# Optimization experiments

Measured on AMD Instinct MI355X. Metric: run time of the kernel, lower is better.

The kernel has to match this reference:

```python
import jax, jax.numpy as jnp
import numpy as np
from jax import lax


def _conv(x, w):
    # x: [B,H,W,C], w: [kh,kw,Cin,Cout], stride 1, 'same' padding
    return lax.conv_general_dilated(x, w, window_strides=(1, 1), padding='SAME',
                                    dimension_numbers=('NHWC', 'HWIO', 'NHWC'))


def setup_inputs() -> dict:
    key = jax.random.key(0)
    ks = jax.random.split(key, 4)
    B, T, H, W, Cin, F = 16, 5, 256, 256, 3, 8
    return {
        'input_tensor': jax.random.normal(ks[0], (B, T, H, W, Cin), jnp.float32),
        'kernel': jax.random.normal(ks[1], (3, 3, Cin, 4 * F), jnp.float32) * 0.1,
        'recurrent_kernel': jax.random.normal(ks[2], (3, 3, F, 4 * F), jnp.float32) * 0.1,
        'bias': jnp.zeros((4 * F,), jnp.float32),
        'gamma': jnp.ones((F,), jnp.float32),
        'beta': jnp.zeros((F,), jnp.float32),
        'moving_mean': jnp.zeros((F,), jnp.float32),
        'moving_var': jnp.ones((F,), jnp.float32),
        'dense_w': jax.random.normal(ks[3], (F, 2), jnp.float32) * 0.1,
        'dense_b': jnp.zeros((2,), jnp.float32),
    }


def reference(input_tensor, kernel, recurrent_kernel, bias, gamma, beta,
              moving_mean, moving_var, dense_w, dense_b):
    B, T, H, W, Cin = input_tensor.shape
    F = recurrent_kernel.shape[2]
    xs = jnp.moveaxis(input_tensor, 1, 0)  # [T,B,H,W,Cin] time-major for scan
    h0 = jnp.zeros((B, H, W, F), input_tensor.dtype)

    def step(carry, x_t):
        h, c = carry
        # fused 4-gate pre-activations, Keras gate order: i, f, c(g), o
        z = _conv(x_t, kernel) + _conv(h, recurrent_kernel) + bias
        i, f, g, o = jnp.split(z, 4, axis=-1)
        i = jax.nn.sigmoid(i)
        f = jax.nn.sigmoid(f)
        g = jnp.tanh(g)
        o = jax.nn.sigmoid(o)
        c = f * c + i * g
        h = o * jnp.tanh(c)
        return (h, c), None

    (h, _), _ = lax.scan(step, (h0, h0), xs)  # return_sequences=False -> last h

    # BatchNormalization (inference, Keras eps=1e-3)
    eps = 1e-3
    x = (h - moving_mean) * lax.rsqrt(moving_var + eps) * gamma + beta
    # LeakyReLU, Keras default alpha=0.3
    x = jnp.where(x >= 0, x, 0.3 * x)
    # Dense(2) over channel dim
    return jnp.einsum('bhwf,fk->bhwk', x, dense_w) + dense_b
```

## Files before the change

### kernel.cpp

```cpp
#include <hip/hip_runtime.h>


#define BB  16
#define TT  5
#define HH  256
#define WW  256
#define CIN 3
#define FF  8
#define GG  32

#define TW  32
#define THT 16
#define LW  34
#define LH  18

typedef _Float16 half8 __attribute__((ext_vector_type(8)));
typedef _Float16 half4 __attribute__((ext_vector_type(4)));
typedef float    floatx4 __attribute__((ext_vector_type(4)));

__device__ __forceinline__ float frcp(float x) { return __builtin_amdgcn_rcpf(x); }
__device__ __forceinline__ float fsig(float x) { return frcp(1.0f + __expf(-x)); }
__device__ __forceinline__ float ftanh_(float x) { return 1.0f - 2.0f * frcp(1.0f + __expf(2.0f * x)); }

#define MFMA(A, B, C) __builtin_amdgcn_mfma_f32_16x16x32_f16((A), (B), (C), 0, 0, 0)

__global__ void build_frags(const float* __restrict__ wk,
                            const float* __restrict__ wr,
                            _Float16* __restrict__ blob) {
    const int lane = threadIdx.x & 63;
    const int quad = lane >> 4, nlo = lane & 15;
    for (int chunk = 0; chunk < 5; ++chunk) {
        for (int nh = 0; nh < 2; ++nh) {
            const int n = nh * 16 + nlo;
            const int frag = chunk * 2 + nh;
            _Float16* dhi = blob + ((size_t)frag * 64 + lane) * 8;
            _Float16* dlo = blob + ((size_t)(10 + frag) * 64 + lane) * 8;
            for (int j = 0; j < 8; ++j) {
                const int k = quad * 8 + j;
                float w = 0.0f;
                if (chunk == 0) {
                    int tap = k >> 2, ci = k & 3;
                    if (ci < 3) w = wk[(tap * 3 + ci) * GG + n];
                } else if (chunk == 1) {
                    if (quad == 0 && j < 3) w = wk[(8 * 3 + j) * GG + n];
                } else {
                    int c = chunk - 2;
                    int tap = c * 4 + quad, ci = j;
                    if (tap < 9) w = wr[(tap * FF + ci) * GG + n];
                }
                _Float16 wh = (_Float16)w;
                dhi[j] = wh;
                dlo[j] = (_Float16)(w - (float)wh);
            }
        }
    }
}

template <bool FIRST>
__global__ __launch_bounds__(256) void lstm_step(
    const float* __restrict__ xg,
    int t,
    const _Float16* __restrict__ blob,
    const float* __restrict__ bias,
    const _Float16* __restrict__ hin,
    _Float16* __restrict__ hout,
    float* __restrict__ cbuf)
{
    __shared__ half8 hls[LH * LW];
    __shared__ half4 xh_ls[LH * LW];
    __shared__ half4 xl_ls[LH * LW];

    const int tid  = threadIdx.x;
    const int bx = blockIdx.x, by = blockIdx.y, b = blockIdx.z;
    const int lane = tid & 63, wave = tid >> 6;
    const int quad = lane >> 4, nlo = lane & 15;

    half8 bfh[10], bfl[10];
#pragma unroll
    for (int i = 0; i < 10; ++i) {
        bfh[i] = *(const half8*)(blob + ((size_t)i * 64 + lane) * 8);
        bfl[i] = *(const half8*)(blob + ((size_t)(10 + i) * 64 + lane) * 8);
    }
    const float bv0 = bias[nlo], bv1 = bias[16 + nlo];

    for (int l = tid; l < LH * LW; l += 256) {
        int r = l / LW, c = l - r * LW;
        int gy = by * THT + r - 1, gx = bx * TW + c - 1;
        half4 vh = {(_Float16)0, (_Float16)0, (_Float16)0, (_Float16)0};
        half4 vl = vh;
        if ((unsigned)gy < HH && (unsigned)gx < WW) {
            const float* p = xg + (((size_t)(b * TT + t) * HH + gy) * WW + gx) * CIN;
#pragma unroll
            for (int ch = 0; ch < 3; ++ch) {
                float xv = p[ch];
                _Float16 xh = (_Float16)xv;
                vh[ch] = xh;
                vl[ch] = (_Float16)(xv - (float)xh);
            }
        }
        xh_ls[l] = vh;
        xl_ls[l] = vl;
    }
    if (!FIRST) {
        for (int l = tid; l < LH * LW; l += 256) {
            int r = l / LW, c = l - r * LW;
            int gy = by * THT + r - 1, gx = bx * TW + c - 1;
            half8 v = {(_Float16)0, (_Float16)0, (_Float16)0, (_Float16)0,
                       (_Float16)0, (_Float16)0, (_Float16)0, (_Float16)0};
            if ((unsigned)gy < HH && (unsigned)gx < WW)
                v = *(const half8*)(hin + ((size_t)(b * HH + gy) * WW + gx) * FF);
            hls[l] = v;
        }
    }
    __syncthreads();

    const int gidbase = (((b * gridDim.y + by) * gridDim.x + bx) * 4 + wave) * 8;

    for (int g = 0; g < 8; ++g) {
        const int lr  = wave * 4 + (g >> 1);
        const int gx0 = (g & 1) * 16;
        const int lc  = gx0 + nlo;

        const int t0 = 2 * quad, t1 = t0 + 1;
        const int i0 = (lr + t0 / 3) * LW + lc + t0 % 3;
        const int i1 = (lr + t1 / 3) * LW + lc + t1 % 3;
        const int i2 = (lr + 2) * LW + lc + 2;
        half8 a_xA_h, a_xB_h, a_xA_l, a_xB_l;
        {
            half4 p = xh_ls[i0], q = xh_ls[i1], s = xh_ls[i2];
            a_xA_h = (half8){p.x, p.y, p.z, p.w, q.x, q.y, q.z, q.w};
            a_xB_h = (half8){s.x, s.y, s.z, s.w, s.x, s.y, s.z, s.w};
        }
        {
            half4 p = xl_ls[i0], q = xl_ls[i1], s = xl_ls[i2];
            a_xA_l = (half8){p.x, p.y, p.z, p.w, q.x, q.y, q.z, q.w};
            a_xB_l = (half8){s.x, s.y, s.z, s.w, s.x, s.y, s.z, s.w};
        }

        floatx4 acc0 = {bv0, bv0, bv0, bv0};
        floatx4 acc1 = {bv1, bv1, bv1, bv1};
        acc0 = MFMA(a_xA_h, bfh[0], acc0);  acc1 = MFMA(a_xA_h, bfh[1], acc1);
        acc0 = MFMA(a_xB_h, bfh[2], acc0);  acc1 = MFMA(a_xB_h, bfh[3], acc1);
        acc0 = MFMA(a_xA_l, bfh[0], acc0);  acc1 = MFMA(a_xA_l, bfh[1], acc1);
        acc0 = MFMA(a_xB_l, bfh[2], acc0);  acc1 = MFMA(a_xB_l, bfh[3], acc1);
        acc0 = MFMA(a_xA_h, bfl[0], acc0);  acc1 = MFMA(a_xA_h, bfl[1], acc1);
        acc0 = MFMA(a_xB_h, bfl[2], acc0);  acc1 = MFMA(a_xB_h, bfl[3], acc1);
        if (!FIRST) {
#pragma unroll
            for (int c = 0; c < 3; ++c) {
                int tap = c * 4 + quad;
                if (tap > 8) tap = 8;
                half8 ah = hls[(lr + tap / 3) * LW + lc + tap % 3];
                acc0 = MFMA(ah, bfh[4 + c * 2], acc0);
                acc1 = MFMA(ah, bfh[5 + c * 2], acc1);
                acc0 = MFMA(ah, bfl[4 + c * 2], acc0);
                acc1 = MFMA(ah, bfl[5 + c * 2], acc1);
            }
        }

        const bool lo8 = (nlo < 8);
        float s0 = lo8 ? acc0[2] : acc0[0]; float r0 = __shfl_xor(s0, 8, 64);
        float s1 = lo8 ? acc0[3] : acc0[1]; float r1 = __shfl_xor(s1, 8, 64);
        float s2 = lo8 ? acc1[2] : acc1[0]; float r2 = __shfl_xor(s2, 8, 64);
        float s3 = lo8 ? acc1[3] : acc1[1]; float r3 = __shfl_xor(s3, 8, 64);

        const float zi0 = lo8 ? acc0[0] : r0, zi1 = lo8 ? acc0[1] : r1;
        const float zf0 = lo8 ? r0 : acc0[2], zf1 = lo8 ? r1 : acc0[3];
        const float zg0 = lo8 ? acc1[0] : r2, zg1 = lo8 ? acc1[1] : r3;
        const float zo0 = lo8 ? r2 : acc1[2], zo1 = lo8 ? r3 : acc1[3];

        float* cp = cbuf + ((size_t)(gidbase + g) * 64 + lane) * 2;
        float c0 = 0.0f, c1 = 0.0f;
        if (!FIRST) { float2 cc = *(const float2*)cp; c0 = cc.x; c1 = cc.y; }

        const float ii0 = fsig(zi0), ff0 = fsig(zf0), gg0 = ftanh_(zg0), oo0 = fsig(zo0);
        const float cn0 = ff0 * c0 + ii0 * gg0;
        const float hn0 = oo0 * ftanh_(cn0);
        const float ii1 = fsig(zi1), ff1 = fsig(zf1), gg1 = ftanh_(zg1), oo1 = fsig(zo1);
        const float cn1 = ff1 * c1 + ii1 * gg1;
        const float hn1 = oo1 * ftanh_(cn1);
        *(float2*)cp = make_float2(cn0, cn1);

        const int fc = nlo & 7;
        const int m0 = quad * 4 + (lo8 ? 0 : 2);
        const int gy = by * THT + lr;
        _Float16* hp = hout + ((size_t)(b * HH + gy) * WW + bx * TW + gx0 + m0) * FF + fc;
        hp[0]  = (_Float16)hn0;
        hp[FF] = (_Float16)hn1;
    }
}

__global__ __launch_bounds__(256) void epilogue_kernel(
    const _Float16* __restrict__ hbuf,
    const float* __restrict__ gamma, const float* __restrict__ beta,
    const float* __restrict__ mean,  const float* __restrict__ var,
    const float* __restrict__ dw,    const float* __restrict__ db,
    float* __restrict__ out)
{
    const size_t p = (size_t)blockIdx.x * 256 + threadIdx.x;
    half8 hv8 = *(const half8*)(hbuf + p * FF);
    float o0 = db[0], o1 = db[1];
#pragma unroll
    for (int f = 0; f < FF; ++f) {
        float s = gamma[f] * rsqrtf(var[f] + 1e-3f);
        float x = ((float)hv8[f] - mean[f]) * s + beta[f];
        x = (x >= 0.f) ? x : 0.3f * x;
        o0 = fmaf(x, dw[f * 2 + 0], o0);
        o1 = fmaf(x, dw[f * 2 + 1], o1);
    }
    *(float2*)(out + p * 2) = make_float2(o0, o1);
}

extern "C" void kernel_launch(void* const* d_in, const int* in_sizes, int n_in,
                              void* d_out, int out_size, void* d_ws, size_t ws_size,
                              hipStream_t stream) {
    const float* x     = (const float*)d_in[0];
    const float* wk    = (const float*)d_in[1];
    const float* wr    = (const float*)d_in[2];
    const float* bias  = (const float*)d_in[3];
    const float* gamma = (const float*)d_in[4];
    const float* beta  = (const float*)d_in[5];
    const float* mean  = (const float*)d_in[6];
    const float* var   = (const float*)d_in[7];
    const float* dw    = (const float*)d_in[8];
    const float* db    = (const float*)d_in[9];
    float* out = (float*)d_out;

    const size_t state = (size_t)BB * HH * WW * FF;
    _Float16* blob = (_Float16*)d_ws;
    float*    cbuf = (float*)((char*)d_ws + 32768);
    _Float16* h0   = (_Float16*)((char*)d_ws + 32768 + state * 4);
    _Float16* h1   = (_Float16*)((char*)h0 + state * 2);

    build_frags<<<1, 64, 0, stream>>>(wk, wr, blob);

    dim3 grid(WW / TW, HH / THT, BB);
    dim3 block(256);
    _Float16* bufs[2] = {h0, h1};
    lstm_step<true><<<grid, block, 0, stream>>>(x, 0, blob, bias, h0 , bufs[1], cbuf);
    for (int t = 1; t < TT; ++t)
        lstm_step<false><<<grid, block, 0, stream>>>(x, t, blob, bias, bufs[t & 1], bufs[(t + 1) & 1], cbuf);

    epilogue_kernel<<<(BB * HH * WW) / 256, 256, 0, stream>>>(
        bufs[TT & 1], gamma, beta, mean, var, dw, db, out);
}
```

Baseline: 276.7 us.

## Fuse all LSTM timesteps and epilogue into one persistent kernel with grid barriers

Replaces the per-timestep kernel launches and the separate epilogue with a single persistent kernel of 512 blocks. Each block owns two 32x32 tiles across all timesteps and synchronises between steps with an atomic grid barrier. The cell state now lives in registers instead of a global buffer, and BN, LeakyReLU and Dense are fused into the last step. It also drops the low-half split of the input x (fp16 only), which removes MFMAs but loses precision, and the co-residency needed by the grid barrier raises register pressure and deadlock risk.

Measured after the change: 989.7 us. 3.58x slower.

```diff
diff --git a/kernel.cpp b/kernel.cpp
--- a/kernel.cpp
+++ b/kernel.cpp
@@ -10,9 +10,11 @@
 #define GG  32
 
 #define TW  32
-#define THT 16
+#define THT 32
 #define LW  34
-#define LH  18
+#define LH  34
+#define NG  16
+#define NBLK 512
 
 typedef _Float16 half8 __attribute__((ext_vector_type(8)));
 typedef _Float16 half4 __attribute__((ext_vector_type(4)));
@@ -56,52 +58,50 @@
     }
 }
 
-template <bool FIRST>
-__global__ __launch_bounds__(256) void lstm_step(
+__device__ __forceinline__ void grid_barrier(unsigned* cnt) {
+    __syncthreads();
+    __threadfence();
+    if (threadIdx.x == 0) {
+        __hip_atomic_fetch_add(cnt, 1u, __ATOMIC_ACQ_REL, __HIP_MEMORY_SCOPE_AGENT);
+        while (__hip_atomic_load(cnt, __ATOMIC_ACQUIRE, __HIP_MEMORY_SCOPE_AGENT)
+               < (unsigned)NBLK)
+            __builtin_amdgcn_s_sleep(8);
+    }
+    __syncthreads();
+    __threadfence();
+}
+
+__device__ __forceinline__ void process_tile(
+    int t, int tile,
     const float* __restrict__ xg,
-    int t,
-    const _Float16* __restrict__ blob,
-    const float* __restrict__ bias,
-    const _Float16* __restrict__ hin,
-    _Float16* __restrict__ hout,
-    float* __restrict__ cbuf)
+    const half8 (&bfh)[10], const half8 (&bfl)[10],
+    float bv0, float bv1,
+    float bn_s, float bn_b, float dw0, float dw1, float db0, float db1,
+    const _Float16* __restrict__ hin, _Float16* __restrict__ hout,
+    float* __restrict__ out,
+    half8* hls, half4* xls,
+    float (&creg)[NG][2])
 {
-    __shared__ half8 hls[LH * LW];
-    __shared__ half4 xh_ls[LH * LW];
-    __shared__ half4 xl_ls[LH * LW];
-
     const int tid  = threadIdx.x;
-    const int bx = blockIdx.x, by = blockIdx.y, b = blockIdx.z;
+    const int b = tile >> 6, by = (tile >> 3) & 7, bx = tile & 7;
     const int lane = tid & 63, wave = tid >> 6;
     const int quad = lane >> 4, nlo = lane & 15;
-
-    half8 bfh[10], bfl[10];
-#pragma unroll
-    for (int i = 0; i < 10; ++i) {
-        bfh[i] = *(const half8*)(blob + ((size_t)i * 64 + lane) * 8);
-        bfl[i] = *(const half8*)(blob + ((size_t)(10 + i) * 64 + lane) * 8);
-    }
-    const float bv0 = bias[nlo], bv1 = bias[16 + nlo];
+    const bool lo8 = (nlo < 8);
+    const int fc = nlo & 7;
+
+    __syncthreads();
 
     for (int l = tid; l < LH * LW; l += 256) {
         int r = l / LW, c = l - r * LW;
         int gy = by * THT + r - 1, gx = bx * TW + c - 1;
         half4 vh = {(_Float16)0, (_Float16)0, (_Float16)0, (_Float16)0};
-        half4 vl = vh;
         if ((unsigned)gy < HH && (unsigned)gx < WW) {
             const float* p = xg + (((size_t)(b * TT + t) * HH + gy) * WW + gx) * CIN;
-#pragma unroll
-            for (int ch = 0; ch < 3; ++ch) {
-                float xv = p[ch];
-                _Float16 xh = (_Float16)xv;
-                vh[ch] = xh;
-                vl[ch] = (_Float16)(xv - (float)xh);
-            }
-        }
-        xh_ls[l] = vh;
-        xl_ls[l] = vl;
-    }
-    if (!FIRST) {
+            vh.x = (_Float16)p[0]; vh.y = (_Float16)p[1]; vh.z = (_Float16)p[2];
+        }
+        xls[l] = vh;
+    }
+    if (t > 0) {
         for (int l = tid; l < LH * LW; l += 256) {
             int r = l / LW, c = l - r * LW;
             int gy = by * THT + r - 1, gx = bx * TW + c - 1;
@@ -114,38 +114,26 @@
     }
     __syncthreads();
 
-    const int gidbase = (((b * gridDim.y + by) * gridDim.x + bx) * 4 + wave) * 8;
-
-    for (int g = 0; g < 8; ++g) {
-        const int lr  = wave * 4 + (g >> 1);
+#pragma unroll
+    for (int g = 0; g < NG; ++g) {
+        const int lr  = wave * 8 + (g >> 1);
         const int gx0 = (g & 1) * 16;
         const int lc  = gx0 + nlo;
 
         const int t0 = 2 * quad, t1 = t0 + 1;
-        const int i0 = (lr + t0 / 3) * LW + lc + t0 % 3;
-        const int i1 = (lr + t1 / 3) * LW + lc + t1 % 3;
-        const int i2 = (lr + 2) * LW + lc + 2;
-        half8 a_xA_h, a_xB_h, a_xA_l, a_xB_l;
-        {
-            half4 p = xh_ls[i0], q = xh_ls[i1], s = xh_ls[i2];
-            a_xA_h = (half8){p.x, p.y, p.z, p.w, q.x, q.y, q.z, q.w};
-            a_xB_h = (half8){s.x, s.y, s.z, s.w, s.x, s.y, s.z, s.w};
-        }
-        {
-            half4 p = xl_ls[i0], q = xl_ls[i1], s = xl_ls[i2];
-            a_xA_l = (half8){p.x, p.y, p.z, p.w, q.x, q.y, q.z, q.w};
-            a_xB_l = (half8){s.x, s.y, s.z, s.w, s.x, s.y, s.z, s.w};
-        }
+        half4 p = xls[(lr + t0 / 3) * LW + lc + t0 % 3];
+        half4 q = xls[(lr + t1 / 3) * LW + lc + t1 % 3];
+        half4 s = xls[(lr + 2) * LW + lc + 2];
+        half8 a_xA = (half8){p.x, p.y, p.z, p.w, q.x, q.y, q.z, q.w};
+        half8 a_xB = (half8){s.x, s.y, s.z, s.w, s.x, s.y, s.z, s.w};
 
         floatx4 acc0 = {bv0, bv0, bv0, bv0};
         floatx4 acc1 = {bv1, bv1, bv1, bv1};
-        acc0 = MFMA(a_xA_h, bfh[0], acc0);  acc1 = MFMA(a_xA_h, bfh[1], acc1);
-        acc0 = MFMA(a_xB_h, bfh[2], acc0);  acc1 = MFMA(a_xB_h, bfh[3], acc1);
-        acc0 = MFMA(a_xA_l, bfh[0], acc0);  acc1 = MFMA(a_xA_l, bfh[1], acc1);
-        acc0 = MFMA(a_xB_l, bfh[2], acc0);  acc1 = MFMA(a_xB_l, bfh[3], acc1);
-        acc0 = MFMA(a_xA_h, bfl[0], acc0);  acc1 = MFMA(a_xA_h, bfl[1], acc1);
-        acc0 = MFMA(a_xB_h, bfl[2], acc0);  acc1 = MFMA(a_xB_h, bfl[3], acc1);
-        if (!FIRST) {
+        acc0 = MFMA(a_xA, bfh[0], acc0);  acc1 = MFMA(a_xA, bfh[1], acc1);
+        acc0 = MFMA(a_xB, bfh[2], acc0);  acc1 = MFMA(a_xB, bfh[3], acc1);
+        acc0 = MFMA(a_xA, bfl[0], acc0);  acc1 = MFMA(a_xA, bfl[1], acc1);
+        acc0 = MFMA(a_xB, bfl[2], acc0);  acc1 = MFMA(a_xB, bfl[3], acc1);
+        if (t > 0) {
 #pragma unroll
             for (int c = 0; c < 3; ++c) {
                 int tap = c * 4 + quad;
@@ -158,7 +146,6 @@
             }
         }
 
-        const bool lo8 = (nlo < 8);
         float s0 = lo8 ? acc0[2] : acc0[0]; float r0 = __shfl_xor(s0, 8, 64);
         float s1 = lo8 ? acc0[3] : acc0[1]; float r1 = __shfl_xor(s1, 8, 64);
         float s2 = lo8 ? acc1[2] : acc1[0]; float r2 = __shfl_xor(s2, 8, 64);
@@ -169,46 +156,92 @@
         const float zg0 = lo8 ? acc1[0] : r2, zg1 = lo8 ? acc1[1] : r3;
         const float zo0 = lo8 ? r2 : acc1[2], zo1 = lo8 ? r3 : acc1[3];
 
-        float* cp = cbuf + ((size_t)(gidbase + g) * 64 + lane) * 2;
-        float c0 = 0.0f, c1 = 0.0f;
-        if (!FIRST) { float2 cc = *(const float2*)cp; c0 = cc.x; c1 = cc.y; }
-
         const float ii0 = fsig(zi0), ff0 = fsig(zf0), gg0 = ftanh_(zg0), oo0 = fsig(zo0);
-        const float cn0 = ff0 * c0 + ii0 * gg0;
+        const float cn0 = ff0 * creg[g][0] + ii0 * gg0;
         const float hn0 = oo0 * ftanh_(cn0);
         const float ii1 = fsig(zi1), ff1 = fsig(zf1), gg1 = ftanh_(zg1), oo1 = fsig(zo1);
-        const float cn1 = ff1 * c1 + ii1 * gg1;
+        const float cn1 = ff1 * creg[g][1] + ii1 * gg1;
         const float hn1 = oo1 * ftanh_(cn1);
-        *(float2*)cp = make_float2(cn0, cn1);
-
-        const int fc = nlo & 7;
+        creg[g][0] = cn0; creg[g][1] = cn1;
+
         const int m0 = quad * 4 + (lo8 ? 0 : 2);
         const int gy = by * THT + lr;
-        _Float16* hp = hout + ((size_t)(b * HH + gy) * WW + bx * TW + gx0 + m0) * FF + fc;
-        hp[0]  = (_Float16)hn0;
-        hp[FF] = (_Float16)hn1;
-    }
-}
-
-__global__ __launch_bounds__(256) void epilogue_kernel(
-    const _Float16* __restrict__ hbuf,
+        if (t < TT - 1) {
+            _Float16* hp = hout + ((size_t)(b * HH + gy) * WW + bx * TW + gx0 + m0) * FF + fc;
+            hp[0]  = (_Float16)hn0;
+            hp[FF] = (_Float16)hn1;
+        } else {
+            float y0 = bn_s * hn0 + bn_b; y0 = (y0 >= 0.f) ? y0 : 0.3f * y0;
+            float y1 = bn_s * hn1 + bn_b; y1 = (y1 >= 0.f) ? y1 : 0.3f * y1;
+            float p00 = y0 * dw0, p01 = y0 * dw1;
+            float p10 = y1 * dw0, p11 = y1 * dw1;
+#pragma unroll
+            for (int m = 1; m <= 4; m <<= 1) {
+                p00 += __shfl_xor(p00, m, 64);
+                p01 += __shfl_xor(p01, m, 64);
+                p10 += __shfl_xor(p10, m, 64);
+                p11 += __shfl_xor(p11, m, 64);
+            }
+            const int j = nlo & 7;
+            if (j < 4) {
+                const int px = m0 + (j >> 1);
+                const int k  = j & 1;
+                float val = (j == 0 ? p00 : j == 1 ? p01 : j == 2 ? p10 : p11)
+                            + (k ? db1 : db0);
+                out[((size_t)(b * HH + gy) * WW + bx * TW + gx0 + px) * 2 + k] = val;
+            }
+        }
+    }
+}
+
+__global__ __launch_bounds__(256, 3) void lstm_all(
+    const float* __restrict__ xg,
+    const _Float16* __restrict__ blob,
+    const float* __restrict__ bias,
     const float* __restrict__ gamma, const float* __restrict__ beta,
     const float* __restrict__ mean,  const float* __restrict__ var,
     const float* __restrict__ dw,    const float* __restrict__ db,
-    float* __restrict__ out)
+    _Float16* __restrict__ h0g, _Float16* __restrict__ h1g,
+    float* __restrict__ out, unsigned* __restrict__ barcnt)
 {
-    const size_t p = (size_t)blockIdx.x * 256 + threadIdx.x;
-    half8 hv8 = *(const half8*)(hbuf + p * FF);
-    float o0 = db[0], o1 = db[1];
-#pragma unroll
-    for (int f = 0; f < FF; ++f) {
-        float s = gamma[f] * rsqrtf(var[f] + 1e-3f);
-        float x = ((float)hv8[f] - mean[f]) * s + beta[f];
-        x = (x >= 0.f) ? x : 0.3f * x;
-        o0 = fmaf(x, dw[f * 2 + 0], o0);
-        o1 = fmaf(x, dw[f * 2 + 1], o1);
-    }
-    *(float2*)(out + p * 2) = make_float2(o0, o1);
+    __shared__ half8 hls[LH * LW];
+    __shared__ half4 xls[LH * LW];
+
+    const int lane = threadIdx.x & 63;
+    const int nlo = lane & 15, fc = nlo & 7;
+
+    half8 bfh[10], bfl[10];
+#pragma unroll
+    for (int i = 0; i < 10; ++i) {
+        bfh[i] = *(const half8*)(blob + ((size_t)i * 64 + lane) * 8);
+        bfl[i] = *(const half8*)(blob + ((size_t)(10 + i) * 64 + lane) * 8);
+    }
+    const float bv0 = bias[nlo], bv1 = bias[16 + nlo];
+    const float bn_s = gamma[fc] * rsqrtf(var[fc] + 1e-3f);
+    const float bn_b = beta[fc] - mean[fc] * bn_s;
+    const float dw0 = dw[fc * 2 + 0], dw1 = dw[fc * 2 + 1];
+    const float db0 = db[0], db1 = db[1];
+
+    float cregA[NG][2], cregB[NG][2];
+#pragma unroll
+    for (int g = 0; g < NG; ++g) {
+        cregA[g][0] = 0.f; cregA[g][1] = 0.f;
+        cregB[g][0] = 0.f; cregB[g][1] = 0.f;
+    }
+
+    for (int t = 0; t < TT; ++t) {
+        const _Float16* hin = (t & 1) ? h0g : h1g;
+        _Float16* hout      = (t & 1) ? h1g : h0g;
+
+        process_tile(t, (int)blockIdx.x, xg, bfh, bfl, bv0, bv1,
+                     bn_s, bn_b, dw0, dw1, db0, db1,
+                     hin, hout, out, hls, xls, cregA);
+        process_tile(t, (int)blockIdx.x + NBLK, xg, bfh, bfl, bv0, bv1,
+                     bn_s, bn_b, dw0, dw1, db0, db1,
+                     hin, hout, out, hls, xls, cregB);
+
+        if (t < TT - 1) grid_barrier(barcnt + t * 16);
+    }
 }
 
 extern "C" void kernel_launch(void* const* d_in, const int* in_sizes, int n_in,
@@ -227,20 +260,14 @@
     float* out = (float*)d_out;
 
     const size_t state = (size_t)BB * HH * WW * FF;
-    _Float16* blob = (_Float16*)d_ws;
-    float*    cbuf = (float*)((char*)d_ws + 32768);
-    _Float16* h0   = (_Float16*)((char*)d_ws + 32768 + state * 4);
-    _Float16* h1   = (_Float16*)((char*)h0 + state * 2);
-
+    _Float16* blob   = (_Float16*)d_ws;
+    unsigned* barcnt = (unsigned*)((char*)d_ws + 24576);
+    _Float16* h0     = (_Float16*)((char*)d_ws + 32768);
+    _Float16* h1     = (_Float16*)((char*)h0 + state * 2);
+
+    hipMemsetAsync((char*)d_ws + 24576, 0, 256, stream);
     build_frags<<<1, 64, 0, stream>>>(wk, wr, blob);
 
-    dim3 grid(WW / TW, HH / THT, BB);
-    dim3 block(256);
-    _Float16* bufs[2] = {h0, h1};
-    lstm_step<true><<<grid, block, 0, stream>>>(x, 0, blob, bias, h0 , bufs[1], cbuf);
-    for (int t = 1; t < TT; ++t)
-        lstm_step<false><<<grid, block, 0, stream>>>(x, t, blob, bias, bufs[t & 1], bufs[(t + 1) & 1], cbuf);
-
-    epilogue_kernel<<<(BB * HH * WW) / 256, 256, 0, stream>>>(
-        bufs[TT & 1], gamma, beta, mean, var, dw, db, out);
-}
+    lstm_all<<<dim3(NBLK), dim3(256), 0, stream>>>(
+        x, blob, bias, gamma, beta, mean, var, dw, db, h0, h1, out, barcnt);
+}
```
